# Kernel optimization log

Measured on AMD Instinct MI355X. Metric: run time of the kernel, lower is better.

Reference implementation:

```python
import jax, jax.numpy as jnp
import numpy as np

B, S, D = 2, 2048, 1024
H = 16
HD = D // H  # 64
SCALE = HD ** -0.5
EPS = 1e-12  # F.normalize eps


def _rope_sin_cos(length, half, dtype):
    positions = jnp.arange(length, dtype=dtype)
    freqs = jnp.arange(half, dtype=dtype)
    inv_freq = 1.0 / 10000 ** (freqs / max(1, half))
    theta = jnp.einsum('s,f->sf', positions, inv_freq)  # [S, half]
    return jnp.sin(theta)[None, None], jnp.cos(theta)[None, None]  # [1,1,S,half]


def _rotate(x, sin, cos):
    # x: [B,H,S,HD]; interleaved even/odd rotation
    x_even = x[..., 0::2]
    x_odd = x[..., 1::2]
    r_even = x_even * cos - x_odd * sin
    r_odd = x_even * sin + x_odd * cos
    return jnp.stack([r_even, r_odd], axis=-1).reshape(x.shape)


def setup_inputs() -> dict:
    key = jax.random.key(0)
    k1, k2, k3 = jax.random.split(key, 3)
    tokens = jax.random.normal(k1, (B, S, D), dtype=jnp.float32)
    qkv_w = jax.random.normal(k2, (3 * D, D), dtype=jnp.float32) * (D ** -0.5)
    qkv_b = jnp.zeros((3 * D,), dtype=jnp.float32)
    out_w = jax.random.normal(k3, (D, D), dtype=jnp.float32) * (D ** -0.5)
    out_b = jnp.zeros((D,), dtype=jnp.float32)
    return {"tokens": tokens, "qkv_w": qkv_w, "qkv_b": qkv_b,
            "out_w": out_w, "out_b": out_b}


def reference(tokens, qkv_w, qkv_b, out_w, out_b):
    batch, length, _ = tokens.shape
    qkv = tokens @ qkv_w.T + qkv_b                       # [B,S,3D]
    qkv = qkv.reshape(batch, length, 3, H, HD)
    qkv = jnp.transpose(qkv, (0, 3, 1, 2, 4))            # [B,H,S,3,HD]
    q, k, v = qkv[..., 0, :], qkv[..., 1, :], qkv[..., 2, :]
    sin, cos = _rope_sin_cos(length, HD // 2, q.dtype)
    q = _rotate(q, sin, cos)
    k = _rotate(k, sin, cos)
    # QK L2-normalize (F.normalize: x / max(||x||, eps))
    q = q / jnp.maximum(jnp.linalg.norm(q, axis=-1, keepdims=True), EPS)
    k = k / jnp.maximum(jnp.linalg.norm(k, axis=-1, keepdims=True), EPS)
    scores = jnp.einsum('bhqd,bhkd->bhqk', q, k) * SCALE
    attn = jax.nn.softmax(scores, axis=-1)
    out = jnp.einsum('bhqk,bhkd->bhqd', attn, v)          # [B,H,S,HD]
    out = jnp.transpose(out, (0, 2, 1, 3)).reshape(batch, length, D)
    return out @ out_w.T + out_b
```

## Files before the change

kernel.cpp:

```cpp
#include <hip/hip_runtime.h>
#include <hip/hip_bf16.h>
#include <math.h>

#define B_ 2
#define S_ 2048
#define D_ 1024
#define H_ 16
#define HD_ 64
#define BHS (B_*H_*S_)
#define NROWS (B_*S_)

typedef __attribute__((ext_vector_type(8))) short bf16x8;
typedef __attribute__((ext_vector_type(4))) short bf16x4;
typedef __attribute__((ext_vector_type(4))) float f32x4;

#ifdef __HIP_DEVICE_COMPILE__
#if __has_builtin(__builtin_amdgcn_mfma_f32_16x16x16bf16_1k)
#define MFMA16(a, b, c) __builtin_amdgcn_mfma_f32_16x16x16bf16_1k(a, b, c, 0, 0, 0)
#else
#define MFMA16(a, b, c) __builtin_amdgcn_mfma_f32_16x16x16_bf16(a, b, c, 0, 0, 0)
#endif
#else
#define MFMA16(a, b, c) (c)
#endif

__device__ __forceinline__ short f2bf(float x) {
  __hip_bfloat16 h = __float2bfloat16(x);
  return *reinterpret_cast<short*>(&h);
}
__device__ __forceinline__ int packbf_hu(float lo, float hi) {
  unsigned lb = __float_as_uint(lo) + 0x8000u;
  unsigned hb = __float_as_uint(hi) + 0x8000u;
  return (int)__builtin_amdgcn_perm(hb, lb, 0x07060302u);
}

__device__ __forceinline__ void gload_lds16(const short* g, short* l) {
  __builtin_amdgcn_global_load_lds(
      (const __attribute__((address_space(1))) void*)g,
      (__attribute__((address_space(3))) void*)l, 16, 0, 0);
}

__global__ __launch_bounds__(256) void prep(
    const float* __restrict__ tokens, const float* __restrict__ qkv_w,
    const float* __restrict__ out_w, short* __restrict__ tok_bf,
    short* __restrict__ qkvw_bf, short* __restrict__ outw_bf,
    float* __restrict__ tab) {
  const int i = blockIdx.x * 256 + threadIdx.x;
  const float* src;
  short* dst;
  int j;
  if (i < 524288) {
    src = tokens; dst = tok_bf; j = i;
  } else if (i < 917504) {
    src = qkv_w; dst = qkvw_bf; j = i - 524288;
  } else if (i < 1048576) {
    src = out_w; dst = outw_bf; j = i - 917504;
  } else if (i < 1056768) {
    const int e = (i - 1048576) * 8;
    const int s = e >> 5;
    const int f0 = e & 31;
#pragma unroll
    for (int k = 0; k < 8; k++) {
      const int f = f0 + k;
      const float theta = (float)s * exp2f(-(float)f * 0.41524101186092034f);
      float sn, cs;
      sincosf(theta, &sn, &cs);
      tab[(s * 32 + f) * 2] = sn;
      tab[(s * 32 + f) * 2 + 1] = cs;
    }
    return;
  } else {
    return;
  }
  const float4 a = *(const float4*)(src + (long)j * 8);
  const float4 b = *(const float4*)(src + (long)j * 8 + 4);
  short tmp[8] = {f2bf(a.x), f2bf(a.y), f2bf(a.z), f2bf(a.w),
                  f2bf(b.x), f2bf(b.y), f2bf(b.z), f2bf(b.w)};
  *(bf16x8*)(dst + (long)j * 8) = *(const bf16x8*)tmp;
}

__global__ __launch_bounds__(256) void qkv_mfma(
    const short* __restrict__ A, const short* __restrict__ W,
    const float* __restrict__ bias, const float* __restrict__ tab,
    short* __restrict__ qb, short* __restrict__ kb, short* __restrict__ vtb) {
  __shared__ short smem[17408];
  short* As = smem;
  short* Bs = smem + 4096;
  const int t = threadIdx.x;
  const int w = t >> 6;
  const int lane = t & 63;
  const int col = lane & 15;
  const int quad = lane >> 4;
  const int wm = w >> 1;
  const int wn = w & 1;
  const int m0 = blockIdx.y * 128;
  const int n0 = blockIdx.x * 128;

  f32x4 acc[4][4] = {};

  for (int k0 = 0; k0 < 1024; k0 += 32) {
    __syncthreads();
#pragma unroll
    for (int i = 0; i < 2; i++) {
      const int c = w * 2 + i;
      const int sl = c * 64 + lane;
      const int row = sl >> 2;
      const int gseg = (sl & 3) ^ (row & 3);
      gload_lds16(&A[(m0 + row) * 1024 + k0 + gseg * 8], As + c * 512);
      gload_lds16(&W[(n0 + row) * 1024 + k0 + gseg * 8], Bs + c * 512);
    }
    __syncthreads();

    bf16x8 af[4], bfr[4];
#pragma unroll
    for (int mt = 0; mt < 4; mt++) {
      const int m = wm * 64 + mt * 16 + col;
      af[mt] = *(const bf16x8*)&As[m * 32 + ((quad ^ (m & 3)) * 8)];
    }
#pragma unroll
    for (int nt = 0; nt < 4; nt++) {
      const int n = wn * 64 + nt * 16 + col;
      bfr[nt] = *(const bf16x8*)&Bs[n * 32 + ((quad ^ (n & 3)) * 8)];
    }
#pragma unroll
    for (int mt = 0; mt < 4; mt++)
#pragma unroll
      for (int nt = 0; nt < 4; nt++)
        acc[mt][nt] = __builtin_amdgcn_mfma_f32_16x16x32_bf16(
            af[mt], bfr[nt], acc[mt][nt], 0, 0, 0);
  }

  const int j_base = n0 + wn * 64;
  const int c = j_base >> 10;
  const int h = (j_base >> 6) & 15;
  float bi[4];
#pragma unroll
  for (int nt = 0; nt < 4; nt++) bi[nt] = bias[j_base + nt * 16 + col];

  if (c < 2) {
    short* dst = (c == 0) ? qb : kb;
#pragma unroll
    for (int mt = 0; mt < 4; mt++) {
#pragma unroll
      for (int r = 0; r < 4; r++) {
        const int n = m0 + wm * 64 + mt * 16 + quad * 4 + r;
        const int bidx = n >> 11;
        const int s = n & 2047;
        float rot[4];
        float ss = 0.0f;
#pragma unroll
        for (int nt = 0; nt < 4; nt++) {
          const float x = acc[mt][nt][r] + bi[nt];
          const int f = (nt * 16 + col) >> 1;
          const float2 sc2 = *(const float2*)&tab[(s * 32 + f) * 2];
          const float partner = __shfl_xor(x, 1, 64);
          rot[nt] = fmaf(partner, (col & 1) ? sc2.x : -sc2.x, x * sc2.y);
          ss += rot[nt] * rot[nt];
        }
        ss += __shfl_xor(ss, 1, 64);
        ss += __shfl_xor(ss, 2, 64);
        ss += __shfl_xor(ss, 4, 64);
        ss += __shfl_xor(ss, 8, 64);
        const float scl = 1.0f / fmaxf(sqrtf(ss), 1e-12f);
        const long base = ((long)(bidx * 16 + h) * 2048 + s) * 64;
#pragma unroll
        for (int nt = 0; nt < 4; nt++)
          dst[base + nt * 16 + col] = f2bf(rot[nt] * scl);
      }
    }
  } else {
    __syncthreads();
    short* T = smem + w * 4352;
#pragma unroll
    for (int mt = 0; mt < 4; mt++)
#pragma unroll
      for (int r = 0; r < 4; r++)
#pragma unroll
        for (int nt = 0; nt < 4; nt++)
          T[(mt * 16 + quad * 4 + r) * 68 + nt * 16 + col] =
              f2bf(acc[mt][nt][r] + bi[nt]);
    const int bidx = (m0 + wm * 64) >> 11;
    const int s0 = (m0 + wm * 64) & 2047;
#pragma unroll
    for (int pass = 0; pass < 4; pass++) {
      const int d = pass * 16 + (lane >> 2);
      const int ks = (lane & 3) * 16;
      short tmp[16];
#pragma unroll
      for (int j = 0; j < 16; j++) tmp[j] = T[(ks + j) * 68 + d];
      short* dstp = vtb + ((long)(bidx * 16 + h) * 64 + d) * 2048 + s0 + ks;
      *(bf16x8*)dstp = *(const bf16x8*)tmp;
      *(bf16x8*)(dstp + 8) = *(const bf16x8*)(tmp + 8);
    }
  }
}

__global__ __launch_bounds__(512) void attn_mfma(
    const short* __restrict__ qb,
    const short* __restrict__ kb,
    const short* __restrict__ vt,
    short* __restrict__ ob) {
  __shared__ __align__(16) char smem[44544];
  short* Kf = (short*)smem;
  short* Vf = (short*)(smem + 16384);
  const int t = threadIdx.x;
  const int w = t >> 6;
  const int grp = w >> 2;
  const int wl = w & 3;
  const int lane = t & 63;
  const int col = lane & 15;
  const int quad = lane >> 4;
  const int bh = blockIdx.x;
  const int q0 = blockIdx.y * 128;
  const long hb = (long)bh * S_ * 64;
  const short* kg = kb + hb;
  const short* vg = vt + (long)bh * 64 * S_;

  bf16x8 qa[2][2];
#pragma unroll
  for (int mt2 = 0; mt2 < 2; mt2++)
#pragma unroll
    for (int h = 0; h < 2; h++)
      qa[mt2][h] = *(const bf16x8*)&qb[hb +
          (long)(q0 + wl * 32 + mt2 * 16 + col) * 64 + h * 32 + quad * 8];

  const int tt = (wl << 6) | lane;
  const int s1 = tt, s2 = tt + 256;
  const int kofs1 = (((s1 >> 7) * 16 + ((s1 >> 2) & 15)) * 64) +
                    ((((s1 >> 6) & 1) * 4 + (s1 & 3)) * 8);
  const int kofs2 = (((s2 >> 7) * 16 + ((s2 >> 2) & 15)) * 64) +
                    ((((s2 >> 6) & 1) * 4 + (s2 & 3)) * 8);
  const int vofs1 = ((s1 >> 7) * 16 + (s1 & 15)) * 2048 + ((s1 >> 4) & 7) * 8;
  const int vofs2 = ((s2 >> 7) * 16 + (s2 & 15)) * 2048 + ((s2 >> 4) & 7) * 8;

  short* KfL = Kf + grp * 4096;
  short* VfL = Vf + grp * 4096;

  f32x4 oacc[2][4] = {};
  float lsum[2] = {0.f, 0.f};

  const int kend = grp * 1024 + 1024;
  for (int kt = grp * 1024; kt < kend; kt += 64) {
    __syncthreads();
    const short* kgp = kg + (long)kt * 64;
    gload_lds16(kgp + kofs1, KfL + wl * 512);
    gload_lds16(kgp + kofs2, KfL + 2048 + wl * 512);
    gload_lds16(vg + kt + vofs1, VfL + wl * 512);
    gload_lds16(vg + kt + vofs2, VfL + 2048 + wl * 512);
    __syncthreads();

#pragma unroll
    for (int nt = 0; nt < 4; nt++) {
      const bf16x8 ka0 = *(const bf16x8*)&KfL[nt * 1024 + col * 32 + quad * 8];
      const bf16x8 ka1 = *(const bf16x8*)&KfL[nt * 1024 + 512 + col * 32 + quad * 8];
      bf16x4 pb[2];
#pragma unroll
      for (int mt2 = 0; mt2 < 2; mt2++) {
        f32x4 z = {0.f, 0.f, 0.f, 0.f};
        z = __builtin_amdgcn_mfma_f32_16x16x32_bf16(ka0, qa[mt2][0], z, 0, 0, 0);
        z = __builtin_amdgcn_mfma_f32_16x16x32_bf16(ka1, qa[mt2][1], z, 0, 0, 0);
        const float e0 = __expf(z[0] * 0.125f);
        const float e1 = __expf(z[1] * 0.125f);
        const float e2 = __expf(z[2] * 0.125f);
        const float e3 = __expf(z[3] * 0.125f);
        lsum[mt2] += (e0 + e1) + (e2 + e3);
        int pk[2] = {packbf_hu(e0, e1), packbf_hu(e2, e3)};
        pb[mt2] = *(const bf16x4*)pk;
      }
      const int c8 = nt * 2 + (quad >> 1);
      const int vb = c8 * 128 + col * 8 + (quad & 1) * 4;
#pragma unroll
      for (int dt = 0; dt < 4; dt++) {
        const bf16x4 va = *(const bf16x4*)&VfL[dt * 1024 + vb];
        oacc[0][dt] = MFMA16(va, pb[0], oacc[0][dt]);
        oacc[1][dt] = MFMA16(va, pb[1], oacc[1][dt]);
      }
    }
  }

  __syncthreads();

#pragma unroll
  for (int mt2 = 0; mt2 < 2; mt2++) {
    float s = lsum[mt2];
    s += __shfl_xor(s, 16, 64);
    s += __shfl_xor(s, 32, 64);
    lsum[mt2] = s;
  }

  float* Ocomb = (float*)smem;
  float* lsumC = (float*)(smem + 34816);
  if (grp == 1) {
#pragma unroll
    for (int mt2 = 0; mt2 < 2; mt2++) {
      const int qloc = wl * 32 + mt2 * 16 + col;
      if (quad == 0) lsumC[qloc] = lsum[mt2];
#pragma unroll
      for (int dt = 0; dt < 4; dt++)
#pragma unroll
        for (int r = 0; r < 4; r++)
          Ocomb[qloc * 68 + dt * 16 + quad * 4 + r] = oacc[mt2][dt][r];
    }
  }
  __syncthreads();
  if (grp == 0) {
    short* T = (short*)(smem + 35328) + wl * 1152;
#pragma unroll
    for (int mt2 = 0; mt2 < 2; mt2++) {
      const int qloc = wl * 32 + mt2 * 16 + col;
      const float inv = 1.0f / (lsum[mt2] + lsumC[qloc]);
#pragma unroll
      for (int dt = 0; dt < 4; dt++)
#pragma unroll
        for (int r = 0; r < 4; r++)
          T[col * 72 + dt * 16 + quad * 4 + r] =
              f2bf((oacc[mt2][dt][r] +
                    Ocomb[qloc * 68 + dt * 16 + quad * 4 + r]) * inv);
      const bf16x8 v0 = *(const bf16x8*)&T[(lane & 15) * 72 + (lane >> 4) * 16];
      const bf16x8 v1 = *(const bf16x8*)&T[(lane & 15) * 72 + (lane >> 4) * 16 + 8];
      short* orow = ob + hb +
          (long)(q0 + wl * 32 + mt2 * 16 + (lane & 15)) * 64 + (lane >> 4) * 16;
      *(bf16x8*)orow = v0;
      *(bf16x8*)(orow + 8) = v1;
    }
  }
}

__global__ __launch_bounds__(256) void out_mfma(
    const short* __restrict__ O, const short* __restrict__ W,
    const float* __restrict__ bias, float* __restrict__ out) {
  __shared__ short As[64 * 32];
  __shared__ short Bs[128 * 32];
  const int t = threadIdx.x;
  const int w = t >> 6;
  const int lane = t & 63;
  const int col = lane & 15;
  const int quad = lane >> 4;
  const int wm = w >> 1;
  const int wn = w & 1;
  const int m0 = blockIdx.y * 64;
  const int n0 = blockIdx.x * 128;

  f32x4 acc[2][4] = {};

  for (int k0 = 0; k0 < 1024; k0 += 32) {
    __syncthreads();
    {
      const int row = t >> 2;
      const int gseg = (t & 3) ^ (row & 3);
      const int n = m0 + row;
      const int bidx = n >> 11;
      const int s = n & 2047;
      const int kk = k0 + gseg * 8;
      gload_lds16(&O[((long)(bidx * 16 + (kk >> 6)) * 2048 + s) * 64 + (kk & 63)],
                  As + w * 512);
    }
#pragma unroll
    for (int i = 0; i < 2; i++) {
      const int cs = w * 2 + i;
      const int sl = cs * 64 + lane;
      const int row = sl >> 2;
      const int gseg = (sl & 3) ^ (row & 3);
      gload_lds16(&W[(n0 + row) * 1024 + k0 + gseg * 8], Bs + cs * 512);
    }
    __syncthreads();

    bf16x8 af[2], bfr[4];
#pragma unroll
    for (int mt = 0; mt < 2; mt++) {
      const int m = wm * 32 + mt * 16 + col;
      af[mt] = *(const bf16x8*)&As[m * 32 + ((quad ^ (m & 3)) * 8)];
    }
#pragma unroll
    for (int nt = 0; nt < 4; nt++) {
      const int n = wn * 64 + nt * 16 + col;
      bfr[nt] = *(const bf16x8*)&Bs[n * 32 + ((quad ^ (n & 3)) * 8)];
    }
#pragma unroll
    for (int mt = 0; mt < 2; mt++)
#pragma unroll
      for (int nt = 0; nt < 4; nt++)
        acc[mt][nt] = __builtin_amdgcn_mfma_f32_16x16x32_bf16(
            af[mt], bfr[nt], acc[mt][nt], 0, 0, 0);
  }

  float bi[4];
#pragma unroll
  for (int nt = 0; nt < 4; nt++) bi[nt] = bias[n0 + wn * 64 + nt * 16 + col];
#pragma unroll
  for (int mt = 0; mt < 2; mt++) {
#pragma unroll
    for (int r = 0; r < 4; r++) {
      const int n = m0 + wm * 32 + mt * 16 + quad * 4 + r;
#pragma unroll
      for (int nt = 0; nt < 4; nt++)
        out[(long)n * 1024 + n0 + wn * 64 + nt * 16 + col] =
            acc[mt][nt][r] + bi[nt];
    }
  }
}

extern "C" void kernel_launch(void* const* d_in, const int* in_sizes, int n_in,
                              void* d_out, int out_size, void* d_ws,
                              size_t ws_size, hipStream_t stream) {
  const float* tokens = (const float*)d_in[0];
  const float* qkv_w = (const float*)d_in[1];
  const float* qkv_b = (const float*)d_in[2];
  const float* out_w = (const float*)d_in[3];
  const float* out_b = (const float*)d_in[4];
  float* out = (float*)d_out;

  const size_t per = (size_t)BHS * HD_;
  float* tab = (float*)d_ws;
  short* tok_bf = (short*)(tab + 2048 * 64);
  short* qkvw_bf = tok_bf + per;
  short* outw_bf = qkvw_bf + 3 * per / 4;
  short* q_bf = outw_bf + per / 4;
  short* k_bf = q_bf + per;
  short* vt_bf = k_bf + per;
  short* O_bf = vt_bf + per;

  hipLaunchKernelGGL(prep, dim3(4128), dim3(256), 0, stream, tokens, qkv_w,
                     out_w, tok_bf, qkvw_bf, outw_bf, tab);
  hipLaunchKernelGGL(qkv_mfma, dim3(24, 32), dim3(256), 0, stream, tok_bf,
                     qkvw_bf, qkv_b, tab, q_bf, k_bf, vt_bf);
  hipLaunchKernelGGL(attn_mfma, dim3(B_ * H_, S_ / 128), dim3(512), 0, stream,
                     q_bf, k_bf, vt_bf, O_bf);
  hipLaunchKernelGGL(out_mfma, dim3(8, 64), dim3(256), 0, stream, O_bf,
                     outw_bf, out_b, out);
}
```

Measured before the change: 214.4 us.

## Pre-tile V and K layouts in QKV epilogue, shrink attention blocks to 64 queries

The QKV epilogue now stages Q/K through shared memory so each lane applies RoPE and L2 normalisation on four contiguous elements and writes packed bf16 pairs. V is written straight from registers in a tiled layout that matches the attention kernel's MFMA fragment order, removing the transpose through shared memory. The attention kernel moves to 256-thread blocks with 64 queries each, doubling the grid, and its K/V loads and final output writes are simplified to match the new layouts. The risk is extra shared-memory staging in the QKV epilogue, and the new tiled V layout has to agree exactly with the attention kernel's reads.

```diff
diff --git a/kernel.cpp b/kernel.cpp
--- a/kernel.cpp
+++ b/kernel.cpp
@@ -137,81 +137,82 @@
 #pragma unroll
   for (int nt = 0; nt < 4; nt++) bi[nt] = bias[j_base + nt * 16 + col];
 
+  __syncthreads();
+
   if (c < 2) {
     short* dst = (c == 0) ? qb : kb;
-#pragma unroll
-    for (int mt = 0; mt < 4; mt++) {
-#pragma unroll
-      for (int r = 0; r < 4; r++) {
-        const int n = m0 + wm * 64 + mt * 16 + quad * 4 + r;
+    float* Tf = (float*)smem + w * 2176;
+#pragma unroll
+    for (int half = 0; half < 2; half++) {
+#pragma unroll
+      for (int mth = 0; mth < 2; mth++) {
+        const int mt = half * 2 + mth;
+#pragma unroll
+        for (int nt = 0; nt < 4; nt++)
+#pragma unroll
+          for (int r = 0; r < 4; r++)
+            Tf[(mth * 16 + quad * 4 + r) * 68 + nt * 16 + col] =
+                acc[mt][nt][r] + bi[nt];
+      }
+#pragma unroll
+      for (int p = 0; p < 8; p++) {
+        const int rloc = p * 4 + quad;
+        const int n = m0 + wm * 64 + half * 32 + rloc;
         const int bidx = n >> 11;
         const int s = n & 2047;
-        float rot[4];
-        float ss = 0.0f;
-#pragma unroll
-        for (int nt = 0; nt < 4; nt++) {
-          const float x = acc[mt][nt][r] + bi[nt];
-          const int f = (nt * 16 + col) >> 1;
-          const float2 sc2 = *(const float2*)&tab[(s * 32 + f) * 2];
-          const float partner = __shfl_xor(x, 1, 64);
-          rot[nt] = fmaf(partner, (col & 1) ? sc2.x : -sc2.x, x * sc2.y);
-          ss += rot[nt] * rot[nt];
-        }
+        const float4 xv = *(const float4*)&Tf[rloc * 68 + col * 4];
+        const float4 tc = *(const float4*)&tab[s * 64 + col * 4];
+        const float e0 = xv.x * tc.y - xv.y * tc.x;
+        const float o0 = xv.x * tc.x + xv.y * tc.y;
+        const float e1 = xv.z * tc.w - xv.w * tc.z;
+        const float o1 = xv.z * tc.z + xv.w * tc.w;
+        float ss = e0 * e0 + o0 * o0 + e1 * e1 + o1 * o1;
         ss += __shfl_xor(ss, 1, 64);
         ss += __shfl_xor(ss, 2, 64);
         ss += __shfl_xor(ss, 4, 64);
         ss += __shfl_xor(ss, 8, 64);
         const float scl = 1.0f / fmaxf(sqrtf(ss), 1e-12f);
-        const long base = ((long)(bidx * 16 + h) * 2048 + s) * 64;
-#pragma unroll
-        for (int nt = 0; nt < 4; nt++)
-          dst[base + nt * 16 + col] = f2bf(rot[nt] * scl);
+        int2 pk;
+        pk.x = packbf_hu(e0 * scl, o0 * scl);
+        pk.y = packbf_hu(e1 * scl, o1 * scl);
+        *(int2*)&dst[((long)(bidx * 16 + h) * 2048 + s) * 64 + col * 4] = pk;
       }
     }
   } else {
-    __syncthreads();
-    short* T = smem + w * 4352;
+    const int n64 = m0 + wm * 64;
+    const int bidx = n64 >> 11;
+    const int st = (n64 & 2047) >> 6;
+    short* vbase = vtb + ((long)(bidx * 16 + h) * 32 + st) * 4096;
 #pragma unroll
     for (int mt = 0; mt < 4; mt++)
 #pragma unroll
-      for (int r = 0; r < 4; r++)
-#pragma unroll
-        for (int nt = 0; nt < 4; nt++)
-          T[(mt * 16 + quad * 4 + r) * 68 + nt * 16 + col] =
-              f2bf(acc[mt][nt][r] + bi[nt]);
-    const int bidx = (m0 + wm * 64) >> 11;
-    const int s0 = (m0 + wm * 64) & 2047;
-#pragma unroll
-    for (int pass = 0; pass < 4; pass++) {
-      const int d = pass * 16 + (lane >> 2);
-      const int ks = (lane & 3) * 16;
-      short tmp[16];
-#pragma unroll
-      for (int j = 0; j < 16; j++) tmp[j] = T[(ks + j) * 68 + d];
-      short* dstp = vtb + ((long)(bidx * 16 + h) * 64 + d) * 2048 + s0 + ks;
-      *(bf16x8*)dstp = *(const bf16x8*)tmp;
-      *(bf16x8*)(dstp + 8) = *(const bf16x8*)(tmp + 8);
-    }
-  }
-}
-
-__global__ __launch_bounds__(512) void attn_mfma(
+      for (int ntq = 0; ntq < 4; ntq++) {
+        int2 pk;
+        pk.x = packbf_hu(acc[mt][ntq][0] + bi[ntq], acc[mt][ntq][1] + bi[ntq]);
+        pk.y = packbf_hu(acc[mt][ntq][2] + bi[ntq], acc[mt][ntq][3] + bi[ntq]);
+        *(int2*)&vbase[((mt * 4 + ntq) * 32 + quad * 8 + (col >> 1)) * 8 +
+                       (col & 1) * 4] = pk;
+      }
+  }
+}
+
+__global__ __launch_bounds__(256) void attn_mfma(
     const short* __restrict__ qb,
     const short* __restrict__ kb,
     const short* __restrict__ vt,
     short* __restrict__ ob) {
-  __shared__ __align__(16) char smem[44544];
+  __shared__ __align__(16) char smem[32768];
   short* Kf = (short*)smem;
-  short* Vf = (short*)(smem + 16384);
+  short* Vf = Kf + 8192;
   const int t = threadIdx.x;
   const int w = t >> 6;
-  const int grp = w >> 2;
-  const int wl = w & 3;
+  const int grp = w >> 1;
+  const int wl = w & 1;
   const int lane = t & 63;
   const int col = lane & 15;
   const int quad = lane >> 4;
   const int bh = blockIdx.x;
-  const int q0 = blockIdx.y * 128;
+  const int q0 = blockIdx.y * 64;
   const long hb = (long)bh * S_ * 64;
   const short* kg = kb + hb;
   const short* vg = vt + (long)bh * 64 * S_;
@@ -225,13 +226,13 @@
           (long)(q0 + wl * 32 + mt2 * 16 + col) * 64 + h * 32 + quad * 8];
 
   const int tt = (wl << 6) | lane;
-  const int s1 = tt, s2 = tt + 256;
-  const int kofs1 = (((s1 >> 7) * 16 + ((s1 >> 2) & 15)) * 64) +
-                    ((((s1 >> 6) & 1) * 4 + (s1 & 3)) * 8);
-  const int kofs2 = (((s2 >> 7) * 16 + ((s2 >> 2) & 15)) * 64) +
-                    ((((s2 >> 6) & 1) * 4 + (s2 & 3)) * 8);
-  const int vofs1 = ((s1 >> 7) * 16 + (s1 & 15)) * 2048 + ((s1 >> 4) & 7) * 8;
-  const int vofs2 = ((s2 >> 7) * 16 + (s2 & 15)) * 2048 + ((s2 >> 4) & 7) * 8;
+  int kofs[4];
+#pragma unroll
+  for (int i = 0; i < 4; i++) {
+    const int cc = tt + 128 * i;
+    kofs[i] = ((cc >> 7) * 16 + (cc & 15)) * 64 + ((cc >> 6) & 1) * 32 +
+              ((cc >> 4) & 3) * 8;
+  }
 
   short* KfL = Kf + grp * 4096;
   short* VfL = Vf + grp * 4096;
@@ -243,16 +244,20 @@
   for (int kt = grp * 1024; kt < kend; kt += 64) {
     __syncthreads();
     const short* kgp = kg + (long)kt * 64;
-    gload_lds16(kgp + kofs1, KfL + wl * 512);
-    gload_lds16(kgp + kofs2, KfL + 2048 + wl * 512);
-    gload_lds16(vg + kt + vofs1, VfL + wl * 512);
-    gload_lds16(vg + kt + vofs2, VfL + 2048 + wl * 512);
+    const short* vgp = vg + (kt >> 6) * 4096;
+#pragma unroll
+    for (int i = 0; i < 4; i++)
+      gload_lds16(kgp + kofs[i], KfL + wl * 512 + i * 1024);
+#pragma unroll
+    for (int i = 0; i < 4; i++)
+      gload_lds16(vgp + tt * 8 + i * 1024, VfL + wl * 512 + i * 1024);
     __syncthreads();
 
 #pragma unroll
     for (int nt = 0; nt < 4; nt++) {
-      const bf16x8 ka0 = *(const bf16x8*)&KfL[nt * 1024 + col * 32 + quad * 8];
-      const bf16x8 ka1 = *(const bf16x8*)&KfL[nt * 1024 + 512 + col * 32 + quad * 8];
+      const bf16x8 ka0 = *(const bf16x8*)&KfL[nt * 1024 + quad * 128 + col * 8];
+      const bf16x8 ka1 =
+          *(const bf16x8*)&KfL[nt * 1024 + 512 + quad * 128 + col * 8];
       bf16x4 pb[2];
 #pragma unroll
       for (int mt2 = 0; mt2 < 2; mt2++) {
@@ -267,11 +272,10 @@
         int pk[2] = {packbf_hu(e0, e1), packbf_hu(e2, e3)};
         pb[mt2] = *(const bf16x4*)pk;
       }
-      const int c8 = nt * 2 + (quad >> 1);
-      const int vb = c8 * 128 + col * 8 + (quad & 1) * 4;
 #pragma unroll
       for (int dt = 0; dt < 4; dt++) {
-        const bf16x4 va = *(const bf16x4*)&VfL[dt * 1024 + vb];
+        const bf16x4 va =
+            *(const bf16x4*)&VfL[(nt * 4 + dt) * 256 + quad * 64 + col * 4];
         oacc[0][dt] = MFMA16(va, pb[0], oacc[0][dt]);
         oacc[1][dt] = MFMA16(va, pb[1], oacc[1][dt]);
       }
@@ -289,7 +293,7 @@
   }
 
   float* Ocomb = (float*)smem;
-  float* lsumC = (float*)(smem + 34816);
+  float* lsumC = (float*)(smem + 17408);
   if (grp == 1) {
 #pragma unroll
     for (int mt2 = 0; mt2 < 2; mt2++) {
@@ -297,31 +301,26 @@
       if (quad == 0) lsumC[qloc] = lsum[mt2];
 #pragma unroll
       for (int dt = 0; dt < 4; dt++)
-#pragma unroll
-        for (int r = 0; r < 4; r++)
-          Ocomb[qloc * 68 + dt * 16 + quad * 4 + r] = oacc[mt2][dt][r];
+        *(f32x4*)&Ocomb[qloc * 68 + dt * 16 + quad * 4] = oacc[mt2][dt];
     }
   }
   __syncthreads();
   if (grp == 0) {
-    short* T = (short*)(smem + 35328) + wl * 1152;
 #pragma unroll
     for (int mt2 = 0; mt2 < 2; mt2++) {
       const int qloc = wl * 32 + mt2 * 16 + col;
       const float inv = 1.0f / (lsum[mt2] + lsumC[qloc]);
-#pragma unroll
-      for (int dt = 0; dt < 4; dt++)
-#pragma unroll
-        for (int r = 0; r < 4; r++)
-          T[col * 72 + dt * 16 + quad * 4 + r] =
-              f2bf((oacc[mt2][dt][r] +
-                    Ocomb[qloc * 68 + dt * 16 + quad * 4 + r]) * inv);
-      const bf16x8 v0 = *(const bf16x8*)&T[(lane & 15) * 72 + (lane >> 4) * 16];
-      const bf16x8 v1 = *(const bf16x8*)&T[(lane & 15) * 72 + (lane >> 4) * 16 + 8];
-      short* orow = ob + hb +
-          (long)(q0 + wl * 32 + mt2 * 16 + (lane & 15)) * 64 + (lane >> 4) * 16;
-      *(bf16x8*)orow = v0;
-      *(bf16x8*)(orow + 8) = v1;
+      short* orow = ob + hb + (long)(q0 + qloc) * 64;
+#pragma unroll
+      for (int dt = 0; dt < 4; dt++) {
+        const float4 oc = *(const float4*)&Ocomb[qloc * 68 + dt * 16 + quad * 4];
+        int2 pk;
+        pk.x = packbf_hu((oacc[mt2][dt][0] + oc.x) * inv,
+                         (oacc[mt2][dt][1] + oc.y) * inv);
+        pk.y = packbf_hu((oacc[mt2][dt][2] + oc.z) * inv,
+                         (oacc[mt2][dt][3] + oc.w) * inv);
+        *(int2*)&orow[dt * 16 + quad * 4] = pk;
+      }
     }
   }
 }
@@ -424,7 +423,7 @@
                      out_w, tok_bf, qkvw_bf, outw_bf, tab);
   hipLaunchKernelGGL(qkv_mfma, dim3(24, 32), dim3(256), 0, stream, tok_bf,
                      qkvw_bf, qkv_b, tab, q_bf, k_bf, vt_bf);
-  hipLaunchKernelGGL(attn_mfma, dim3(B_ * H_, S_ / 128), dim3(512), 0, stream,
+  hipLaunchKernelGGL(attn_mfma, dim3(B_ * H_, S_ / 64), dim3(256), 0, stream,
                      q_bf, k_bf, vt_bf, O_bf);
   hipLaunchKernelGGL(out_mfma, dim3(8, 64), dim3(256), 0, stream, O_bf,
                      outw_bf, out_b, out);
```

Result: slower. 221.2 us (+3.2%).
